# Kernel tuning notes

Measured on AMD Instinct MI355X. Metric: run time of the kernel, lower is better.

## Reference

```python
import jax, jax.numpy as jnp
import numpy as np

D = 2048
N_HEAD = 16
HEAD_DIM = D // N_HEAD
B = 2
T = 2048


def setup_inputs() -> dict:
    key = jax.random.key(0)
    kx, kw1, kb1, kw2, kb2 = jax.random.split(key, 5)
    x = jax.random.normal(kx, (B, T, D), dtype=jnp.float32)
    # causal mask: 1 where attention allowed, 0 where masked
    mask = jnp.tril(jnp.ones((T, T), dtype=jnp.int32))[None, None, :, :]
    s1 = 1.0 / np.sqrt(D)
    Wqkv = jax.random.uniform(kw1, (D, 3 * D), jnp.float32, -s1, s1)
    bqkv = jax.random.uniform(kb1, (3 * D,), jnp.float32, -s1, s1)
    Wproj = jax.random.uniform(kw2, (D, D), jnp.float32, -s1, s1)
    bproj = jax.random.uniform(kb2, (D,), jnp.float32, -s1, s1)
    return {"x": x, "mask": mask, "Wqkv": Wqkv, "bqkv": bqkv,
            "Wproj": Wproj, "bproj": bproj}


def _rope(q, k, seq_len, head_dim):
    # q, k: [B, h, T, head_dim]
    half = head_dim // 2
    idx = jnp.arange(half, dtype=jnp.float32)
    pos = jnp.arange(seq_len, dtype=jnp.float32)[:, None]  # [T,1]
    rates = jnp.power(10000.0, -2.0 * idx / head_dim)      # [half]
    theta = pos * rates                                     # [T, half]
    cos = jnp.cos(theta)
    sin = jnp.sin(theta)

    def apply(x):
        x1 = x[..., :half]
        x2 = x[..., half:half * 2]
        return jnp.concatenate([x1 * cos - x2 * sin, x1 * sin + x2 * cos], axis=-1)

    return apply(q), apply(k)


def reference(x, mask, Wqkv, bqkv, Wproj, bproj):
    Bc, Tc, C = x.shape
    h = N_HEAD
    hd = HEAD_DIM
    qkv = x @ Wqkv + bqkv                      # [B, T, 3C]
    q, k, v = jnp.split(qkv, 3, axis=-1)
    q = q.reshape(Bc, Tc, h, hd).transpose(0, 2, 1, 3)  # [B, h, T, hd]
    k = k.reshape(Bc, Tc, h, hd).transpose(0, 2, 1, 3)
    v = v.reshape(Bc, Tc, h, hd).transpose(0, 2, 1, 3)
    q, k = _rope(q, k, Tc, hd)
    att = jnp.einsum('bhqd,bhkd->bhqk', q, k) * (hd ** -0.5)
    att = jnp.where(mask == 0, -jnp.inf, att)
    att = jax.nn.softmax(att, axis=-1)
    y = jnp.einsum('bhqk,bhkd->bhqd', att, v)  # [B, h, T, hd]
    y = y.transpose(0, 2, 1, 3).reshape(Bc, Tc, C)
    y = y @ Wproj + bproj
    return y
```

## Files before the change

### kernel.cpp

```cpp
#include <hip/hip_runtime.h>
#include <hip/hip_bf16.h>
#include <stdint.h>
#include <stddef.h>

typedef __bf16 bf16;
typedef __attribute__((ext_vector_type(8))) __bf16 bf16x8;
typedef __attribute__((ext_vector_type(4))) __bf16 bf16x4;
typedef __attribute__((ext_vector_type(4))) float f32x4;

#define DM 2048
#define NH 16
#define HDD 128
#define BB 2
#define TT 2048
#define MM (BB*TT)
#define NQKV (3*DM)

#define L2E 1.4426950408889634f
#define ATT_SCALE 0.08838834764831845f
#define NEG_INF (-__builtin_inff())

static_assert(sizeof(bf16x8) == 16, "bf16x8 must be 16B");

#define SB0() __builtin_amdgcn_sched_barrier(0)
#define WAITV0() { asm volatile("s_waitcnt vmcnt(0)" ::: "memory"); SB0(); }
#define WAITL0() { asm volatile("s_waitcnt lgkmcnt(0)" ::: "memory"); SB0(); }
#define BARRIER8() { SB0(); __builtin_amdgcn_s_barrier(); SB0(); }

static __device__ __forceinline__ void gload_lds16(const void* g, void* l) {
  __builtin_amdgcn_global_load_lds(
      (__attribute__((address_space(1))) void*)g,
      (__attribute__((address_space(3))) void*)l, 16, 0, 0);
}

__global__ __launch_bounds__(256) void rope_table_k(float* __restrict__ cT,
                                                    float* __restrict__ sT) {
  int id = blockIdx.x * 256 + threadIdx.x;
  int t = id >> 6, i = id & 63;
  float freq = powf(10000.0f, -(float)i * (1.0f / 64.0f));
  float theta = (float)t * freq;
  float s, c;
  __sincosf(theta, &s, &c);
  cT[id] = c;
  sT[id] = s;
}

__global__ __launch_bounds__(256) void convert_x_k(const float* __restrict__ x,
                                                   bf16* __restrict__ xb) {
  size_t id = (size_t)blockIdx.x * 256 + threadIdx.x;
  size_t o = id * 8;
  float4 a = *(const float4*)(x + o);
  float4 b = *(const float4*)(x + o + 4);
  bf16x8 r;
  r[0] = (bf16)a.x; r[1] = (bf16)a.y; r[2] = (bf16)a.z; r[3] = (bf16)a.w;
  r[4] = (bf16)b.x; r[5] = (bf16)b.y; r[6] = (bf16)b.z; r[7] = (bf16)b.w;
  *(bf16x8*)(xb + o) = r;
}

__global__ __launch_bounds__(256) void transpose_w_k(const float* __restrict__ W,
                                                     bf16* __restrict__ Wt,
                                                     int K, int N) {
  __shared__ float tile[64][65];
  int n0 = blockIdx.x * 64, k0 = blockIdx.y * 64;
  int t = threadIdx.x;
#pragma unroll
  for (int i = 0; i < 16; ++i) {
    int idx = t + i * 256;
    int r = idx >> 6, c = idx & 63;
    tile[r][c] = W[(size_t)(k0 + r) * N + n0 + c];
  }
  __syncthreads();
#pragma unroll
  for (int i = 0; i < 16; ++i) {
    int idx = t + i * 256;
    int r = idx >> 6, c = idx & 63;
    Wt[(size_t)(n0 + r) * K + k0 + c] = (bf16)tile[c][r];
  }
}

__global__ __launch_bounds__(256) void rope_apply_k(bf16* __restrict__ buf,
                                                    const float* __restrict__ cT,
                                                    const float* __restrict__ sT) {
  int id = blockIdx.x * 256 + threadIdx.x;
  int i4 = id & 15;
  int t = (id >> 4) & 2047;
  int bh = id >> 15;
  int idx0 = i4 * 4;
  size_t base = ((size_t)bh * TT + t) * HDD;
  bf16x4 x1 = *(const bf16x4*)(buf + base + idx0);
  bf16x4 x2 = *(const bf16x4*)(buf + base + 64 + idx0);
  float4 ct = *(const float4*)(cT + t * 64 + idx0);
  float4 st = *(const float4*)(sT + t * 64 + idx0);
  bf16x4 o1, o2;
  float c0, s0, a, b2;
#pragma unroll
  for (int j = 0; j < 4; ++j) {
    c0 = (j == 0) ? ct.x : (j == 1) ? ct.y : (j == 2) ? ct.z : ct.w;
    s0 = (j == 0) ? st.x : (j == 1) ? st.y : (j == 2) ? st.z : st.w;
    a = (float)x1[j];
    b2 = (float)x2[j];
    o1[j] = (bf16)(a * c0 - b2 * s0);
    o2[j] = (bf16)(a * s0 + b2 * c0);
  }
  *(bf16x4*)(buf + base + idx0) = o1;
  *(bf16x4*)(buf + base + 64 + idx0) = o2;
}

template <int EPI>
__global__ __launch_bounds__(256, 2) void gemm_bt_k(
    const bf16* __restrict__ A, const bf16* __restrict__ Bt,
    const float* __restrict__ bias,
    bf16* __restrict__ q_out, bf16* __restrict__ k_out, bf16* __restrict__ v_out,
    float* __restrict__ c_out, int M, int N, int K) {
  __shared__ __align__(16) bf16 Asm[128 * 64];
  __shared__ __align__(16) bf16 Bsm[128 * 64];
  const int tid = threadIdx.x;
  const int w = tid >> 6, l = tid & 63;
  const int lane16 = l & 15, lgrp = l >> 4;
  const int wm = w >> 1, wn = w & 1;

  int flat = blockIdx.y * gridDim.x + blockIdx.x;
  {
    const int nwg = gridDim.x * gridDim.y;
    const int cpx = nwg >> 3;
    flat = (flat & 7) * cpx + (flat >> 3);
  }
  const int bm = flat % gridDim.x;
  const int bn = flat / gridDim.x;

  const int l8r = l >> 3, l8c = l & 7;

  f32x4 acc[4][4] = {};

  for (int k0 = 0; k0 < K; k0 += 64) {
    __syncthreads();
#pragma unroll
    for (int i = 0; i < 4; ++i) {
      int slot = w * 4 + i;
      int row = slot * 8 + l8r;
      gload_lds16(A + (size_t)(bm * 128 + row) * K + k0 + l8c * 8,
                  &Asm[slot * 512]);
      gload_lds16(Bt + (size_t)(bn * 128 + row) * K + k0 + l8c * 8,
                  &Bsm[slot * 512]);
    }
    __syncthreads();
#pragma unroll
    for (int kk = 0; kk < 2; ++kk) {
      bf16x8 af[4], bfr[4];
#pragma unroll
      for (int mf = 0; mf < 4; ++mf) {
        int row = wm * 64 + mf * 16 + lane16;
        af[mf] = *(const bf16x8*)&Asm[row * 64 + kk * 32 + lgrp * 8];
      }
#pragma unroll
      for (int nf = 0; nf < 4; ++nf) {
        int col = wn * 64 + nf * 16 + lane16;
        bfr[nf] = *(const bf16x8*)&Bsm[col * 64 + kk * 32 + lgrp * 8];
      }
#pragma unroll
      for (int mf = 0; mf < 4; ++mf)
#pragma unroll
        for (int nf = 0; nf < 4; ++nf)
          acc[mf][nf] = __builtin_amdgcn_mfma_f32_16x16x32_bf16(
              af[mf], bfr[nf], acc[mf][nf], 0, 0, 0);
    }
  }

  if (EPI == 0) {
    const int which = bn >> 4;
    const int head = bn & 15;
    bf16* outb = (which == 0) ? q_out : (which == 1 ? k_out : v_out);
#pragma unroll
    for (int nf = 0; nf < 4; ++nf) {
      int hd = wn * 64 + nf * 16 + lane16;
      float bv = bias[bn * 128 + hd];
#pragma unroll
      for (int mf = 0; mf < 4; ++mf)
#pragma unroll
        for (int r = 0; r < 4; ++r) {
          int row = bm * 128 + wm * 64 + mf * 16 + lgrp * 4 + r;
          int b = row >> 11, t = row & 2047;
          outb[((size_t)(b * NH + head) * TT + t) * HDD + hd] =
              (bf16)(acc[mf][nf][r] + bv);
        }
    }
  } else {
#pragma unroll
    for (int nf = 0; nf < 4; ++nf) {
      int colg = bn * 128 + wn * 64 + nf * 16 + lane16;
      float bv = bias[colg];
#pragma unroll
      for (int mf = 0; mf < 4; ++mf)
#pragma unroll
        for (int r = 0; r < 4; ++r) {
          int row = bm * 128 + wm * 64 + mf * 16 + lgrp * 4 + r;
          c_out[(size_t)row * N + colg] = acc[mf][nf][r] + bv;
        }
    }
  }
}

#define MFMA_Q(MF0, NF0, NCNT)                                             \
  do {                                                                     \
    __builtin_amdgcn_s_setprio(1);                                         \
    _Pragma("unroll") for (int mf = 0; mf < 4; ++mf)                       \
    _Pragma("unroll") for (int nf = 0; nf < (NCNT); ++nf)                  \
    _Pragma("unroll") for (int kk = 0; kk < 2; ++kk)                       \
      acc[(MF0) + mf][(NF0) + nf] = __builtin_amdgcn_mfma_f32_16x16x32_bf16( \
          af[(MF0) + mf][kk], bfr[(NF0) + nf][kk], acc[(MF0) + mf][(NF0) + nf], 0, 0, 0); \
    __builtin_amdgcn_s_setprio(0);                                         \
  } while (0)

__global__ __launch_bounds__(512, 2) void gemm8_qkv_k(
    const bf16* __restrict__ A, const bf16* __restrict__ Bt,
    const float* __restrict__ bias,
    bf16* __restrict__ q_out, bf16* __restrict__ k_out, bf16* __restrict__ v_out,
    int M, int N, int K) {
  __shared__ __align__(16) char Lsm[2][57344];
  const int tid = threadIdx.x;
  const int wid = tid >> 6, l = tid & 63;
  const int lane16 = l & 15, lgrp = l >> 4;
  const int wm = wid >> 2, wn = wid & 3;

  int flat = blockIdx.y * gridDim.x + blockIdx.x;
  {
    const int cpx = (gridDim.x * gridDim.y) >> 3;
    flat = (flat & 7) * cpx + (flat >> 3);
  }
  const int bm = flat % gridDim.x;
  const int bn = flat / gridDim.x;
  const int NT = K >> 6;

  const int schunk = (l & 7) ^ ((l >> 3) & 7);
  const bf16* gA = A + (size_t)(bm * 256 + wid * 8 + (l >> 3)) * K + schunk * 8;
  const bf16* gB = Bt + (size_t)(bn * 192 + wid * 8 + (l >> 3)) * K + schunk * 8;

  auto stage_unit = [&](int mat, int t, int u, int buf) {
    const bf16* g = (mat ? gB : gA) + (size_t)(u * 64) * K + t * 64;
    gload_lds16(g, &Lsm[buf][(mat ? 32768 : 0) + u * 8192 + wid * 1024]);
  };

  f32x4 acc[8][3] = {};

#pragma unroll
  for (int u = 0; u < 4; ++u) stage_unit(0, 0, u, 0);
#pragma unroll
  for (int u = 0; u < 3; ++u) stage_unit(1, 0, u, 0);

  for (int t = 0; t < NT; ++t) {
    const int cur = t & 1;
    const char* As = &Lsm[cur][0];
    const char* Bs = &Lsm[cur][32768];
    bf16x8 af[8][2], bfr[3][2];

    WAITV0();
    BARRIER8();

#pragma unroll
    for (int mf = 0; mf < 4; ++mf)
#pragma unroll
      for (int kk = 0; kk < 2; ++kk) {
        int row = wm * 128 + mf * 16 + lane16;
        int ch = (kk * 4 + lgrp) ^ (lane16 & 7);
        af[mf][kk] = *(const bf16x8*)(As + row * 128 + ch * 16);
      }
#pragma unroll
    for (int nf = 0; nf < 2; ++nf)
#pragma unroll
      for (int kk = 0; kk < 2; ++kk) {
        int row = wn * 48 + nf * 16 + lane16;
        int ch = (kk * 4 + lgrp) ^ (lane16 & 7);
        bfr[nf][kk] = *(const bf16x8*)(Bs + row * 128 + ch * 16);
      }
    if (t + 1 < NT) {
#pragma unroll
      for (int u = 0; u < 4; ++u) stage_unit(0, t + 1, u, cur ^ 1);
    }
    WAITL0();
    MFMA_Q(0, 0, 2);
    BARRIER8();

#pragma unroll
    for (int mf = 4; mf < 8; ++mf)
#pragma unroll
      for (int kk = 0; kk < 2; ++kk) {
        int row = wm * 128 + mf * 16 + lane16;
        int ch = (kk * 4 + lgrp) ^ (lane16 & 7);
        af[mf][kk] = *(const bf16x8*)(As + row * 128 + ch * 16);
      }
#pragma unroll
    for (int kk = 0; kk < 2; ++kk) {
      int row = wn * 48 + 32 + lane16;
      int ch = (kk * 4 + lgrp) ^ (lane16 & 7);
      bfr[2][kk] = *(const bf16x8*)(Bs + row * 128 + ch * 16);
    }
    if (t + 1 < NT) {
#pragma unroll
      for (int u = 0; u < 3; ++u) stage_unit(1, t + 1, u, cur ^ 1);
    }
    WAITL0();
    MFMA_Q(0, 2, 1);
    BARRIER8();

    MFMA_Q(4, 0, 2);
    BARRIER8();

    MFMA_Q(4, 2, 1);
  }

#pragma unroll
  for (int nf = 0; nf < 3; ++nf) {
    int colg = bn * 192 + wn * 48 + nf * 16 + lane16;
    int which = colg >> 11;
    bf16* outb = (which == 0) ? q_out : (which == 1 ? k_out : v_out);
    int head = (colg >> 7) & 15, hd = colg & 127;
    float bv = bias[colg];
#pragma unroll
    for (int mf = 0; mf < 8; ++mf)
#pragma unroll
      for (int r = 0; r < 4; ++r) {
        int row = bm * 256 + wm * 128 + mf * 16 + lgrp * 4 + r;
        int bb = row >> 11, tt2 = row & 2047;
        outb[((size_t)(bb * NH + head) * TT + tt2) * HDD + hd] =
            (bf16)(acc[mf][nf][r] + bv);
      }
  }
}

__global__ __launch_bounds__(512, 2) void attn_k(
    const bf16* __restrict__ Q, const bf16* __restrict__ Kt,
    const bf16* __restrict__ V, bf16* __restrict__ Y) {
  __shared__ __align__(16) bf16 Ksm[128 * 128];
  __shared__ __align__(16) bf16 Vsm[128 * 128];
  __shared__ __align__(16) bf16 Psm[8][16 * 128];
  const int tid = threadIdx.x, w = tid >> 6, l = tid & 63;
  const int lane16 = l & 15, lgrp = l >> 4;
  const int bh = blockIdx.y;
  const int b = bh >> 4, h = bh & 15;
  const size_t base = (size_t)bh * TT * HDD;

  uint4 vreg[4];
  const int vg = tid >> 4, vh8 = tid & 15;

  auto load_V = [&](int k0) {
#pragma unroll
    for (int kq = 0; kq < 4; ++kq)
      vreg[kq] = *(const uint4*)(V + base + (size_t)(k0 + vg * 4 + kq) * HDD + vh8 * 8);
  };
  auto issue_K = [&](int k0) {
#pragma unroll
    for (int i = 0; i < 4; ++i) {
      int key = w * 16 + i * 4 + (l >> 4);
      int c = (l & 15) ^ ((key ^ (key >> 3)) & 15);
      gload_lds16(Kt + base + (size_t)(k0 + key) * HDD + c * 8,
                  &Ksm[(w * 16 + i * 4) * 128 + (l & 15) * 8]);
    }
  };
  auto write_V = [&]() {
    const unsigned* dw = (const unsigned*)vreg;
    int hd0 = vh8 * 8;
#pragma unroll
    for (int j = 0; j < 8; ++j) {
      int ww = j >> 1;
      unsigned sel = (j & 1) ? 0x07060302u : 0x05040100u;
      uint2 val;
      val.x = __builtin_amdgcn_perm(dw[4 + ww], dw[0 + ww], sel);
      val.y = __builtin_amdgcn_perm(dw[12 + ww], dw[8 + ww], sel);
      int hd = hd0 + j;
      int ch = (vg >> 1) ^ ((hd ^ (hd >> 3)) & 15);
      *(uint2*)((char*)Vsm + hd * 256 + (ch << 4) + ((vg & 1) << 3)) = val;
    }
  };

  for (int pass = 0; pass < 2; ++pass) {
    const int qt = (pass == 0) ? (int)blockIdx.x : 15 - (int)blockIdx.x;
    const int q0 = qt * 128;
    const int nt = qt + 1;

    bf16x8 qa[4];
    {
      int row = q0 + w * 16 + lane16;
#pragma unroll
      for (int kk = 0; kk < 4; ++kk)
        qa[kk] = *(const bf16x8*)(Q + base + (size_t)row * HDD + kk * 32 + lgrp * 8);
    }

    f32x4 o[8] = {};
    float m_r[4], l_r[4];
#pragma unroll
    for (int r = 0; r < 4; ++r) { m_r[r] = NEG_INF; l_r[r] = 0.f; }

    for (int kt = 0; kt < nt; ++kt) {
      const int k0 = kt * 128;
      load_V(k0);
      issue_K(k0);
      write_V();
      __syncthreads();

      f32x4 s[8] = {};
#pragma unroll
      for (int kk = 0; kk < 4; ++kk) {
#pragma unroll
        for (int nf = 0; nf < 8; ++nf) {
          int key = nf * 16 + lane16;
          int ch = (kk * 4 + lgrp) ^ ((key ^ (key >> 3)) & 15);
          bf16x8 kf = *(const bf16x8*)((char*)Ksm + key * 256 + (ch << 4));
          s[nf] = __builtin_amdgcn_mfma_f32_16x16x32_bf16(
              qa[kk], kf, s[nf], 0, 0, 0);
        }
      }

      const int rowbase = q0 + w * 16 + lgrp * 4;
      const bool needmask = (k0 + 127 > q0 + w * 16);
#pragma unroll
      for (int nf = 0; nf < 8; ++nf) {
        int col = k0 + nf * 16 + lane16;
#pragma unroll
        for (int r = 0; r < 4; ++r) {
          float sv = s[nf][r] * ATT_SCALE;
          if (needmask && col > rowbase + r) sv = -3.0e38f;
          s[nf][r] = sv;
        }
      }

#pragma unroll
      for (int r = 0; r < 4; ++r) {
        float tm = fmaxf(fmaxf(fmaxf(s[0][r], s[1][r]), fmaxf(s[2][r], s[3][r])),
                         fmaxf(fmaxf(s[4][r], s[5][r]), fmaxf(s[6][r], s[7][r])));
        tm = fmaxf(tm, __shfl_xor(tm, 1));
        tm = fmaxf(tm, __shfl_xor(tm, 2));
        tm = fmaxf(tm, __shfl_xor(tm, 4));
        tm = fmaxf(tm, __shfl_xor(tm, 8));
        float mo = m_r[r];
        float mn = fmaxf(mo, tm);
        float alpha = exp2f((mo - mn) * L2E);
        m_r[r] = mn;
        float rs = 0.f;
#pragma unroll
        for (int nf = 0; nf < 8; ++nf) {
          float p = exp2f((s[nf][r] - mn) * L2E);
          s[nf][r] = p;
          rs += p;
        }
        rs += __shfl_xor(rs, 1);
        rs += __shfl_xor(rs, 2);
        rs += __shfl_xor(rs, 4);
        rs += __shfl_xor(rs, 8);
        l_r[r] = l_r[r] * alpha + rs;
#pragma unroll
        for (int nf = 0; nf < 8; ++nf) o[nf][r] *= alpha;
      }

#pragma unroll
      for (int nf = 0; nf < 8; ++nf)
#pragma unroll
        for (int r = 0; r < 4; ++r) {
          int rl = lgrp * 4 + r;
          int ch = (2 * nf + (lane16 >> 3)) ^ ((rl ^ (rl >> 3)) & 15);
          int byte = rl * 256 + (ch << 4) + ((lane16 & 7) << 1);
          *(bf16*)((char*)&Psm[w][0] + byte) = (bf16)s[nf][r];
        }
      bf16x8 pa[4];
#pragma unroll
      for (int kk = 0; kk < 4; ++kk) {
        int ch = (kk * 4 + lgrp) ^ ((lane16 ^ (lane16 >> 3)) & 15);
        pa[kk] = *(const bf16x8*)((char*)&Psm[w][0] + lane16 * 256 + (ch << 4));
      }

#pragma unroll
      for (int nf = 0; nf < 8; ++nf) {
#pragma unroll
        for (int kk = 0; kk < 4; ++kk) {
          int hd = nf * 16 + lane16;
          int ch = (kk * 4 + lgrp) ^ ((hd ^ (hd >> 3)) & 15);
          bf16x8 vf = *(const bf16x8*)((char*)Vsm + hd * 256 + (ch << 4));
          o[nf] = __builtin_amdgcn_mfma_f32_16x16x32_bf16(
              pa[kk], vf, o[nf], 0, 0, 0);
        }
      }

      __syncthreads();
    }

#pragma unroll
    for (int r = 0; r < 4; ++r) {
      float inv = 1.0f / l_r[r];
      int row = q0 + w * 16 + lgrp * 4 + r;
#pragma unroll
      for (int nf = 0; nf < 8; ++nf) {
        int hd = nf * 16 + lane16;
        Y[(size_t)(b * TT + row) * DM + h * HDD + hd] = (bf16)(o[nf][r] * inv);
      }
    }
  }
}

extern "C" void kernel_launch(void* const* d_in, const int* in_sizes, int n_in,
                              void* d_out, int out_size, void* d_ws, size_t ws_size,
                              hipStream_t stream) {
  const float* x = (const float*)d_in[0];
  const float* Wqkv = (const float*)d_in[2];
  const float* bqkv = (const float*)d_in[3];
  const float* Wproj = (const float*)d_in[4];
  const float* bproj = (const float*)d_in[5];
  float* out = (float*)d_out;

  char* ws = (char*)d_ws;
  bf16* xb = (bf16*)ws;                 ws += (size_t)MM * DM * 2;
  bf16* Wqkvt = (bf16*)ws;              ws += (size_t)NQKV * DM * 2;
  bf16* Wprojt = (bf16*)ws;             ws += (size_t)DM * DM * 2;
  bf16* kb = (bf16*)ws;                 ws += (size_t)MM * DM * 2;
  bf16* vb = (bf16*)ws;                 ws += (size_t)MM * DM * 2;
  float* cosT = (float*)ws;             ws += (size_t)TT * 64 * 4;
  float* sinT = (float*)ws;             ws += (size_t)TT * 64 * 4;
  bf16* qb = (bf16*)d_out;
  bf16* yb = xb;

  rope_table_k<<<dim3(512), dim3(256), 0, stream>>>(cosT, sinT);
  convert_x_k<<<dim3(4096), dim3(256), 0, stream>>>(x, xb);
  transpose_w_k<<<dim3(96, 32), dim3(256), 0, stream>>>(Wqkv, Wqkvt, DM, NQKV);
  transpose_w_k<<<dim3(32, 32), dim3(256), 0, stream>>>(Wproj, Wprojt, DM, DM);

  gemm8_qkv_k<<<dim3(16, 32), dim3(512), 0, stream>>>(
      xb, Wqkvt, bqkv, qb, kb, vb, MM, NQKV, DM);

  rope_apply_k<<<dim3(4096), dim3(256), 0, stream>>>(qb, cosT, sinT);
  rope_apply_k<<<dim3(4096), dim3(256), 0, stream>>>(kb, cosT, sinT);

  attn_k<<<dim3(8, 32), dim3(512), 0, stream>>>(qb, kb, vb, yb);

  gemm_bt_k<1><<<dim3(32, 16), dim3(256), 0, stream>>>(
      yb, Wprojt, bproj, nullptr, nullptr, nullptr, out, MM, DM, DM);
}
```

Measured before the change: 297.7 us.

## Replace projection GEMM with double-buffered swizzled 256x128 tile kernel

Replaces the simple single-buffered 128x128 output projection GEMM with an 8-wave 256x128 tile kernel. The new kernel uses double-buffered LDS with prefetch of the next K tile interleaved between MFMA quarters, plus XOR-swizzled LDS chunks to avoid bank conflicts. It reuses the pipelined structure of the QKV GEMM. The aim is to hide global load latency and raise MFMA utilisation, at the cost of more LDS per block and fewer workgroups (256 vs 512).

New measurement: 285.7 us. 1.04x faster.

```diff
diff --git a/kernel.cpp b/kernel.cpp
--- a/kernel.cpp
+++ b/kernel.cpp
@@ -106,100 +106,6 @@
   *(bf16x4*)(buf + base + 64 + idx0) = o2;
 }
 
-template <int EPI>
-__global__ __launch_bounds__(256, 2) void gemm_bt_k(
-    const bf16* __restrict__ A, const bf16* __restrict__ Bt,
-    const float* __restrict__ bias,
-    bf16* __restrict__ q_out, bf16* __restrict__ k_out, bf16* __restrict__ v_out,
-    float* __restrict__ c_out, int M, int N, int K) {
-  __shared__ __align__(16) bf16 Asm[128 * 64];
-  __shared__ __align__(16) bf16 Bsm[128 * 64];
-  const int tid = threadIdx.x;
-  const int w = tid >> 6, l = tid & 63;
-  const int lane16 = l & 15, lgrp = l >> 4;
-  const int wm = w >> 1, wn = w & 1;
-
-  int flat = blockIdx.y * gridDim.x + blockIdx.x;
-  {
-    const int nwg = gridDim.x * gridDim.y;
-    const int cpx = nwg >> 3;
-    flat = (flat & 7) * cpx + (flat >> 3);
-  }
-  const int bm = flat % gridDim.x;
-  const int bn = flat / gridDim.x;
-
-  const int l8r = l >> 3, l8c = l & 7;
-
-  f32x4 acc[4][4] = {};
-
-  for (int k0 = 0; k0 < K; k0 += 64) {
-    __syncthreads();
-#pragma unroll
-    for (int i = 0; i < 4; ++i) {
-      int slot = w * 4 + i;
-      int row = slot * 8 + l8r;
-      gload_lds16(A + (size_t)(bm * 128 + row) * K + k0 + l8c * 8,
-                  &Asm[slot * 512]);
-      gload_lds16(Bt + (size_t)(bn * 128 + row) * K + k0 + l8c * 8,
-                  &Bsm[slot * 512]);
-    }
-    __syncthreads();
-#pragma unroll
-    for (int kk = 0; kk < 2; ++kk) {
-      bf16x8 af[4], bfr[4];
-#pragma unroll
-      for (int mf = 0; mf < 4; ++mf) {
-        int row = wm * 64 + mf * 16 + lane16;
-        af[mf] = *(const bf16x8*)&Asm[row * 64 + kk * 32 + lgrp * 8];
-      }
-#pragma unroll
-      for (int nf = 0; nf < 4; ++nf) {
-        int col = wn * 64 + nf * 16 + lane16;
-        bfr[nf] = *(const bf16x8*)&Bsm[col * 64 + kk * 32 + lgrp * 8];
-      }
-#pragma unroll
-      for (int mf = 0; mf < 4; ++mf)
-#pragma unroll
-        for (int nf = 0; nf < 4; ++nf)
-          acc[mf][nf] = __builtin_amdgcn_mfma_f32_16x16x32_bf16(
-              af[mf], bfr[nf], acc[mf][nf], 0, 0, 0);
-    }
-  }
-
-  if (EPI == 0) {
-    const int which = bn >> 4;
-    const int head = bn & 15;
-    bf16* outb = (which == 0) ? q_out : (which == 1 ? k_out : v_out);
-#pragma unroll
-    for (int nf = 0; nf < 4; ++nf) {
-      int hd = wn * 64 + nf * 16 + lane16;
-      float bv = bias[bn * 128 + hd];
-#pragma unroll
-      for (int mf = 0; mf < 4; ++mf)
-#pragma unroll
-        for (int r = 0; r < 4; ++r) {
-          int row = bm * 128 + wm * 64 + mf * 16 + lgrp * 4 + r;
-          int b = row >> 11, t = row & 2047;
-          outb[((size_t)(b * NH + head) * TT + t) * HDD + hd] =
-              (bf16)(acc[mf][nf][r] + bv);
-        }
-    }
-  } else {
-#pragma unroll
-    for (int nf = 0; nf < 4; ++nf) {
-      int colg = bn * 128 + wn * 64 + nf * 16 + lane16;
-      float bv = bias[colg];
-#pragma unroll
-      for (int mf = 0; mf < 4; ++mf)
-#pragma unroll
-        for (int r = 0; r < 4; ++r) {
-          int row = bm * 128 + wm * 64 + mf * 16 + lgrp * 4 + r;
-          c_out[(size_t)row * N + colg] = acc[mf][nf][r] + bv;
-        }
-    }
-  }
-}
-
 #define MFMA_Q(MF0, NF0, NCNT)                                             \
   do {                                                                     \
     __builtin_amdgcn_s_setprio(1);                                         \
@@ -323,6 +229,110 @@
         int bb = row >> 11, tt2 = row & 2047;
         outb[((size_t)(bb * NH + head) * TT + tt2) * HDD + hd] =
             (bf16)(acc[mf][nf][r] + bv);
+      }
+  }
+}
+
+__global__ __launch_bounds__(512, 2) void gemm4_proj_k(
+    const bf16* __restrict__ A, const bf16* __restrict__ Bt,
+    const float* __restrict__ bias, float* __restrict__ c_out,
+    int M, int N, int K) {
+  __shared__ __align__(16) char Lsm[2][49152];
+  const int tid = threadIdx.x;
+  const int wid = tid >> 6, l = tid & 63;
+  const int lane16 = l & 15, lgrp = l >> 4;
+  const int wm = wid >> 2, wn = wid & 3;
+
+  int flat = blockIdx.y * gridDim.x + blockIdx.x;
+  {
+    const int cpx = (gridDim.x * gridDim.y) >> 3;
+    flat = (flat & 7) * cpx + (flat >> 3);
+  }
+  const int bm = flat % gridDim.x;
+  const int bn = flat / gridDim.x;
+  const int NT = K >> 6;
+
+  const int schunk = (l & 7) ^ ((l >> 3) & 7);
+  const bf16* gA = A + (size_t)(bm * 256 + wid * 8 + (l >> 3)) * K + schunk * 8;
+  const bf16* gB = Bt + (size_t)(bn * 128 + wid * 8 + (l >> 3)) * K + schunk * 8;
+
+  auto stage_unit = [&](int mat, int t, int u, int buf) {
+    const bf16* g = (mat ? gB : gA) + (size_t)(u * 64) * K + t * 64;
+    gload_lds16(g, &Lsm[buf][(mat ? 32768 : 0) + u * 8192 + wid * 1024]);
+  };
+
+  f32x4 acc[8][2] = {};
+
+#pragma unroll
+  for (int u = 0; u < 4; ++u) stage_unit(0, 0, u, 0);
+#pragma unroll
+  for (int u = 0; u < 2; ++u) stage_unit(1, 0, u, 0);
+
+  for (int t = 0; t < NT; ++t) {
+    const int cur = t & 1;
+    const char* As = &Lsm[cur][0];
+    const char* Bs = &Lsm[cur][32768];
+    bf16x8 af[8][2], bfr[2][2];
+
+    WAITV0();
+    BARRIER8();
+
+#pragma unroll
+    for (int mf = 0; mf < 4; ++mf)
+#pragma unroll
+      for (int kk = 0; kk < 2; ++kk) {
+        int row = wm * 128 + mf * 16 + lane16;
+        int ch = (kk * 4 + lgrp) ^ (lane16 & 7);
+        af[mf][kk] = *(const bf16x8*)(As + row * 128 + ch * 16);
+      }
+#pragma unroll
+    for (int nf = 0; nf < 2; ++nf)
+#pragma unroll
+      for (int kk = 0; kk < 2; ++kk) {
+        int row = wn * 32 + nf * 16 + lane16;
+        int ch = (kk * 4 + lgrp) ^ (lane16 & 7);
+        bfr[nf][kk] = *(const bf16x8*)(Bs + row * 128 + ch * 16);
+      }
+    if (t + 1 < NT) {
+#pragma unroll
+      for (int u = 0; u < 4; ++u) stage_unit(0, t + 1, u, cur ^ 1);
+    }
+    WAITL0();
+    MFMA_Q(0, 0, 1);
+    BARRIER8();
+
+#pragma unroll
+    for (int mf = 4; mf < 8; ++mf)
+#pragma unroll
+      for (int kk = 0; kk < 2; ++kk) {
+        int row = wm * 128 + mf * 16 + lane16;
+        int ch = (kk * 4 + lgrp) ^ (lane16 & 7);
+        af[mf][kk] = *(const bf16x8*)(As + row * 128 + ch * 16);
+      }
+    if (t + 1 < NT) {
+#pragma unroll
+      for (int u = 0; u < 2; ++u) stage_unit(1, t + 1, u, cur ^ 1);
+    }
+    WAITL0();
+    MFMA_Q(0, 1, 1);
+    BARRIER8();
+
+    MFMA_Q(4, 0, 1);
+    BARRIER8();
+
+    MFMA_Q(4, 1, 1);
+  }
+
+#pragma unroll
+  for (int nf = 0; nf < 2; ++nf) {
+    int colg = bn * 128 + wn * 32 + nf * 16 + lane16;
+    float bv = bias[colg];
+#pragma unroll
+    for (int mf = 0; mf < 8; ++mf)
+#pragma unroll
+      for (int r = 0; r < 4; ++r) {
+        int row = bm * 256 + wm * 128 + mf * 16 + lgrp * 4 + r;
+        c_out[(size_t)row * N + colg] = acc[mf][nf][r] + bv;
       }
   }
 }
@@ -529,6 +539,6 @@
 
   attn_k<<<dim3(8, 32), dim3(512), 0, stream>>>(qb, kb, vb, yb);
 
-  gemm_bt_k<1><<<dim3(32, 16), dim3(256), 0, stream>>>(
-      yb, Wprojt, bproj, nullptr, nullptr, nullptr, out, MM, DM, DM);
-}
+  gemm4_proj_k<<<dim3(16, 16), dim3(512), 0, stream>>>(
+      yb, Wprojt, bproj, out, MM, DM, DM);
+}
```
